# Performance work log

Hardware: AMD Instinct MI355X
Metric: run time of the kernel (lower is better)

## Reference

```python
import jax, jax.numpy as jnp
import numpy as np

SAMPLE_RATE = 48000.0
WIN_SIZE = 512   # also the FFT size (nfft = win_size in forward)
HOP_SIZE = 256   # win_size // 2, COLA with Hann
B = 128
NUM_FREQ_PTS = 96000  # 2 s RIR at 48 kHz


def _hann(n):
    # torch.hann_window default is periodic: 0.5*(1 - cos(2*pi*k/n))
    k = jnp.arange(n, dtype=jnp.float32)
    return 0.5 * (1.0 - jnp.cos(2.0 * jnp.pi * k / n))


def _stft(x, win, nfft, hop):
    # x: [B, L] real. center=False, onesided=True, not normalized.
    L = x.shape[-1]
    pad = (-L) % hop  # pad to multiple of hop, as in get_stft_torch
    if pad:
        x = jnp.pad(x, ((0, 0), (0, pad)))
    T = (x.shape[-1] - nfft) // hop + 1  # number of frames
    idx = hop * jnp.arange(T)[:, None] + jnp.arange(nfft)[None, :]  # [T, nfft]
    frames = x[:, idx] * win  # [B, T, nfft]
    return jnp.fft.rfft(frames, n=nfft, axis=-1)  # [B, T, F], F = nfft//2 + 1


def _edr_db(S):
    # S: [B, T, F] complex. EDR[m] = sum_{t>=m} |S[t]|^2  -> reverse cumsum (O(T)).
    P = jnp.abs(S) ** 2  # [B, T, F]
    edr = jnp.flip(jnp.cumsum(jnp.flip(P, axis=1), axis=1), axis=1)
    return 10.0 * jnp.log10(edr)  # db(..., is_squared=True)


def reference(target_re, target_im, ach_re, ach_im):
    n = target_re.shape[-1]
    target_rir = jnp.fft.irfft(target_re + 1j * target_im, n=n)
    ach_rir = jnp.fft.irfft(ach_re + 1j * ach_im, n=n)
    win = _hann(WIN_SIZE)
    S_t = _stft(target_rir, win, WIN_SIZE, HOP_SIZE)
    S_a = _stft(ach_rir, win, WIN_SIZE, HOP_SIZE)
    edr_t = _edr_db(S_t)
    edr_a = _edr_db(S_a)
    return jnp.sum(jnp.abs(edr_t - edr_a)) / jnp.sum(jnp.abs(edr_t))


def setup_inputs() -> dict:
    key = jax.random.key(0)
    k1, k2, k3, k4 = jax.random.split(key, 4)
    shape = (B, NUM_FREQ_PTS)
    return {
        "target_re": jax.random.normal(k1, shape, dtype=jnp.float32),
        "target_im": jax.random.normal(k2, shape, dtype=jnp.float32),
        "ach_re": jax.random.normal(k3, shape, dtype=jnp.float32),
        "ach_im": jax.random.normal(k4, shape, dtype=jnp.float32),
    }
```

## Files before the change

kernel.cpp:

```cpp
#include <hip/hip_runtime.h>
#include <math.h>

#define BATCH   128
#define NFREQ   96000
#define M_HALF  48000
#define NFRAMES 374
#define NBINS   257
#define NG      11
#define GLEN    34
#define FPW     4

#define CS1 246
#define CS2 206

#define PI_D 3.14159265358979323846

#define WAVE_SYNC() __asm__ volatile("s_waitcnt lgkmcnt(0)" ::: "memory")

__device__ __forceinline__ float2 cmulf(float2 a, float2 b) {
  return make_float2(a.x * b.x - a.y * b.y, a.x * b.y + a.y * b.x);
}

__device__ __forceinline__ void bfly4(float2 z0, float2 z1, float2 z2, float2 z3,
                                      float2& o0, float2& o1, float2& o2, float2& o3) {
  float2 e0 = make_float2(z0.x + z2.x, z0.y + z2.y);
  float2 e1 = make_float2(z0.x - z2.x, z0.y - z2.y);
  float2 e2 = make_float2(z1.x + z3.x, z1.y + z3.y);
  float2 e3 = make_float2(z1.x - z3.x, z1.y - z3.y);
  o0 = make_float2(e0.x + e2.x, e0.y + e2.y);
  o2 = make_float2(e0.x - e2.x, e0.y - e2.y);
  o1 = make_float2(e1.x + e3.y, e1.y - e3.x);
  o3 = make_float2(e1.x - e3.y, e1.y + e3.x);
}

__device__ __forceinline__ void bfly4i(float2 z0, float2 z1, float2 z2, float2 z3,
                                       float2& o0, float2& o1, float2& o2, float2& o3) {
  float2 e0 = make_float2(z0.x + z2.x, z0.y + z2.y);
  float2 e1 = make_float2(z0.x - z2.x, z0.y - z2.y);
  float2 e2 = make_float2(z1.x + z3.x, z1.y + z3.y);
  float2 e3 = make_float2(z1.x - z3.x, z1.y - z3.y);
  o0 = make_float2(e0.x + e2.x, e0.y + e2.y);
  o2 = make_float2(e0.x - e2.x, e0.y - e2.y);
  o1 = make_float2(e1.x - e3.y, e1.y + e3.x);
  o3 = make_float2(e1.x + e3.y, e1.y - e3.x);
}

#define PIDX(i) ((i) + ((i) >> 3))

__global__ void setup_kernel(float2* __restrict__ Wm, float2* __restrict__ Wpack,
                             float2* __restrict__ W512, float* __restrict__ hann,
                             float2* __restrict__ W240, float2* __restrict__ W200) {
  int i = blockIdx.x * blockDim.x + threadIdx.x;
  if (i < M_HALF) {
    double th = 2.0 * PI_D * (double)i / (double)M_HALF;
    double s, c; sincos(th, &s, &c);
    Wm[i] = make_float2((float)c, (float)s);
    double th2 = PI_D * (double)i / (double)M_HALF;
    double s2, c2; sincos(th2, &s2, &c2);
    Wpack[i] = make_float2((float)c2, (float)s2);
  }
  if (i < 512) {
    double th = -2.0 * PI_D * (double)i / 512.0;
    double s, c; sincos(th, &s, &c);
    W512[i] = make_float2((float)c, (float)s);
    hann[i] = (float)(0.5 * (1.0 - cos(2.0 * PI_D * (double)i / 512.0)));
  }
  if (i < 240) {
    double th = 2.0 * PI_D * (double)i / 240.0;
    double s, c; sincos(th, &s, &c);
    W240[i] = make_float2((float)c, (float)s);
  }
  if (i < 200) {
    double th = 2.0 * PI_D * (double)i / 200.0;
    double s, c; sincos(th, &s, &c);
    W200[i] = make_float2((float)c, (float)s);
  }
}

__global__ __launch_bounds__(256) void packT_kernel(
    const float* __restrict__ tre, const float* __restrict__ tim,
    const float* __restrict__ are, const float* __restrict__ aim,
    float2* __restrict__ Zt, const float2* __restrict__ Wpack, int b0, int c) {
  __shared__ float dRe[1600], dIm[1600], mRe[1600], mIm[1600];
  const int tid = threadIdx.x;
  const int row = blockIdx.y;
  const int base = blockIdx.x * 1600;
  const int isA = row >= c;
  const int b = b0 + (isA ? row - c : row);
  const float* rr = (isA ? are : tre) + (size_t)b * NFREQ;
  const float* ii = (isA ? aim : tim) + (size_t)b * NFREQ;
  for (int j = tid; j < 1600; j += 256) {
    dRe[j] = rr[base + j];
    dIm[j] = ii[base + j];
    int mk = M_HALF - base - j;
    mRe[j] = rr[mk];
    mIm[j] = ii[mk];
  }
  __syncthreads();
  const float sc = 1.0f / (float)M_HALF;
  float2* Zrow = Zt + (size_t)row * M_HALF;
  const int k2base = blockIdx.x * 8;
  for (int e = tid; e < 1600; e += 256) {
    int k1 = e >> 3, k2o = e & 7;
    int j = k1 + 200 * k2o;
    int k = base + j;
    float xr = dRe[j], xi = dIm[j];
    float yr = mRe[j], yi = mIm[j];
    if (k == 0) { xi = 0.f; yi = 0.f; }
    float Er = 0.5f * (xr + yr);
    float Ei = 0.5f * (xi - yi);
    float Dr = 0.5f * (xr - yr);
    float Di = 0.5f * (xi + yi);
    float2 wp = Wpack[k];
    float tr = wp.x * Dr - wp.y * Di;
    float ti = wp.x * Di + wp.y * Dr;
    Zrow[k1 * 240 + k2base + k2o] = make_float2((Er - ti) * sc, (Ei + tr) * sc);
  }
}

__global__ __launch_bounds__(256) void k1_kernel(
    const float2* __restrict__ Zt, float2* __restrict__ G,
    const float2* __restrict__ Wm, const float2* __restrict__ W240) {
  __shared__ float2 LA[8 * CS1];
  __shared__ float2 LB[8 * CS1];
  const int tid = threadIdx.x;
  const int row = blockIdx.y;
  const int K0 = blockIdx.x * 8;

  {
    const float2* Zrow = Zt + (size_t)row * M_HALF + (size_t)K0 * 240;
    for (int j = tid; j < 8 * 240; j += 256) {
      int col = j / 240, k2 = j - col * 240;
      LA[col * CS1 + k2] = Zrow[j];
    }
  }
  __syncthreads();
  for (int e = tid; e < 8 * 60; e += 256) {
    int col = e & 7, p = e >> 3;
    const float2* in = LA + col * CS1;
    float2 o0, o1, o2, o3;
    bfly4i(in[p], in[p + 60], in[p + 120], in[p + 180], o0, o1, o2, o3);
    o1 = cmulf(o1, W240[p]);
    o2 = cmulf(o2, W240[2 * p]);
    o3 = cmulf(o3, W240[3 * p]);
    float2* out = LB + col * CS1 + 4 * p;
    out[0] = o0; out[1] = o1; out[2] = o2; out[3] = o3;
  }
  __syncthreads();
  for (int e = tid; e < 8 * 60; e += 256) {
    int col = e & 7, t = e >> 3;
    int q = t & 3, p = t >> 2;
    const float2* in = LB + col * CS1;
    float2 o0, o1, o2, o3;
    bfly4i(in[q + 4 * p], in[q + 4 * (p + 15)], in[q + 4 * (p + 30)],
           in[q + 4 * (p + 45)], o0, o1, o2, o3);
    o1 = cmulf(o1, W240[4 * p]);
    o2 = cmulf(o2, W240[8 * p]);
    o3 = cmulf(o3, W240[12 * p]);
    float2* out = LA + col * CS1 + q;
    out[4 * (4 * p + 0)] = o0; out[4 * (4 * p + 1)] = o1;
    out[4 * (4 * p + 2)] = o2; out[4 * (4 * p + 3)] = o3;
  }
  __syncthreads();
  {
    float2 w15[15];
#pragma unroll
    for (int m = 0; m < 15; ++m) w15[m] = W240[16 * m];
    for (int e = tid; e < 8 * 16; e += 256) {
      int col = e & 7, q = e >> 3;
      const float2* in = LA + col * CS1 + q;
      float2 a[15];
#pragma unroll
      for (int j = 0; j < 15; ++j) a[j] = in[16 * j];
      float2* out = LB + col * CS1 + q;
#pragma unroll
      for (int u = 0; u < 15; ++u) {
        float2 acc = a[0];
#pragma unroll
        for (int j = 1; j < 15; ++j) {
          float2 w = w15[(u * j) % 15];
          acc.x += a[j].x * w.x - a[j].y * w.y;
          acc.y += a[j].x * w.y + a[j].y * w.x;
        }
        out[16 * u] = acc;
      }
    }
  }
  __syncthreads();
  {
    const int col = tid & 7;
    const int k1 = K0 + col;
    int n2 = tid >> 3;
    float2 tw = Wm[k1 * n2];
    const float2 twstep = Wm[32 * k1];
    float2* Grow = G + (size_t)row * M_HALF;
    const float2* in = LB + col * CS1;
    for (; n2 < 240; n2 += 32) {
      Grow[(size_t)n2 * 200 + k1] = cmulf(in[n2], tw);
      tw = cmulf(tw, twstep);
    }
  }
}

__global__ __launch_bounds__(256) void k2_kernel(
    const float2* __restrict__ G, float2* __restrict__ X,
    const float2* __restrict__ W200) {
  __shared__ float2 LA[8 * CS2];
  __shared__ float2 LB[8 * CS2];
  const int tid = threadIdx.x;
  const int row = blockIdx.y;
  const int N20 = blockIdx.x * 8;
  const float2* Grow = G + (size_t)row * M_HALF;

  for (int e = tid; e < 8 * 200; e += 256) {
    int n2o = e / 200;
    int k1 = e - n2o * 200;
    LA[n2o * CS2 + k1] = Grow[(size_t)(N20 + n2o) * 200 + k1];
  }
  __syncthreads();
  for (int e = tid; e < 8 * 50; e += 256) {
    int col = e & 7, p = e >> 3;
    const float2* in = LA + col * CS2;
    float2 o0, o1, o2, o3;
    bfly4i(in[p], in[p + 50], in[p + 100], in[p + 150], o0, o1, o2, o3);
    o1 = cmulf(o1, W200[p]);
    o2 = cmulf(o2, W200[2 * p]);
    o3 = cmulf(o3, W200[3 * p]);
    float2* out = LB + col * CS2 + 4 * p;
    out[0] = o0; out[1] = o1; out[2] = o2; out[3] = o3;
  }
  __syncthreads();
  {
    float2 w5[5];
#pragma unroll
    for (int m = 0; m < 5; ++m) w5[m] = W200[40 * m];
    for (int e = tid; e < 8 * 40; e += 256) {
      int col = e & 7, t = e >> 3;
      int q = t & 3, p = t >> 2;
      const float2* in = LB + col * CS2 + q;
      float2 a[5];
#pragma unroll
      for (int j = 0; j < 5; ++j) a[j] = in[4 * (p + 10 * j)];
      float2* out = LA + col * CS2 + q;
#pragma unroll
      for (int u = 0; u < 5; ++u) {
        float2 acc = a[0];
#pragma unroll
        for (int j = 1; j < 5; ++j) {
          float2 w = w5[(u * j) % 5];
          acc.x += a[j].x * w.x - a[j].y * w.y;
          acc.y += a[j].x * w.y + a[j].y * w.x;
        }
        acc = cmulf(acc, W200[4 * u * p]);
        out[4 * (5 * p + u)] = acc;
      }
    }
  }
  __syncthreads();
  {
    float2 w10[10];
#pragma unroll
    for (int m = 0; m < 10; ++m) w10[m] = W200[20 * m];
    for (int e = tid; e < 8 * 20; e += 256) {
      int col = e & 7, q = e >> 3;
      const float2* in = LA + col * CS2 + q;
      float2 a[10];
#pragma unroll
      for (int j = 0; j < 10; ++j) a[j] = in[20 * j];
      float2* out = LB + col * CS2 + q;
#pragma unroll
      for (int u = 0; u < 10; ++u) {
        float2 acc = a[0];
#pragma unroll
        for (int j = 1; j < 10; ++j) {
          float2 w = w10[(u * j) % 10];
          acc.x += a[j].x * w.x - a[j].y * w.y;
          acc.y += a[j].x * w.y + a[j].y * w.x;
        }
        out[20 * u] = acc;
      }
    }
  }
  __syncthreads();
  {
    const int n2o = tid & 7;
    float2* Xrow = X + (size_t)row * M_HALF + (N20 + n2o);
    const float2* in = LB + n2o * CS2;
    for (int n1 = tid >> 3; n1 < 200; n1 += 32)
      Xrow[240 * n1] = in[n1];
  }
}

__global__ __launch_bounds__(256) void stft256_kernel(
    const float* __restrict__ xtime, float* __restrict__ P,
    const float2* __restrict__ W512, const float* __restrict__ hann) {
  __shared__ float2 lds[4][2][288];
  const int tid = threadIdx.x;
  const int wave = tid >> 6;
  const int l = tid & 63;
  const int row = blockIdx.y;
  const int frame0 = (blockIdx.x * 4 + wave) * FPW;

  float2* Abuf = lds[wave][0];
  float2* Bbuf = lds[wave][1];

  const float2* hann2 = (const float2*)hann;
  float2 hw[4];
#pragma unroll
  for (int j = 0; j < 4; ++j) hw[j] = hann2[l + 64 * j];
  float2 t1[3], t2[3], t3[3];
  {
    int p2 = l >> 2, p3 = l >> 4;
#pragma unroll
    for (int u = 1; u <= 3; ++u) {
      t1[u - 1] = W512[2 * u * l];
      t2[u - 1] = W512[8 * u * p2];
      t3[u - 1] = W512[32 * u * p3];
    }
  }

  const float2* xrow = (const float2*)xtime + (size_t)row * 48000;

  for (int fi = 0; fi < FPW; ++fi) {
    const int fr = frame0 + fi;
    const bool active = (fr < NFRAMES);
    float2 z[4];
    if (active) {
      const float2* src = xrow + fr * 128;
#pragma unroll
      for (int j = 0; j < 4; ++j) {
        float2 v = src[l + 64 * j];
        z[j] = make_float2(v.x * hw[j].x, v.y * hw[j].y);
      }
    } else {
#pragma unroll
      for (int j = 0; j < 4; ++j) z[j] = make_float2(0.f, 0.f);
    }
    float2 o0, o1, o2, o3;
    bfly4(z[0], z[1], z[2], z[3], o0, o1, o2, o3);
    o1 = cmulf(o1, t1[0]); o2 = cmulf(o2, t1[1]); o3 = cmulf(o3, t1[2]);
    Abuf[PIDX(4 * l + 0)] = o0; Abuf[PIDX(4 * l + 1)] = o1;
    Abuf[PIDX(4 * l + 2)] = o2; Abuf[PIDX(4 * l + 3)] = o3;
    WAVE_SYNC();
    {
      int q = l & 3, p = l >> 2;
      float2 a0 = Abuf[PIDX(q + 4 * p)];
      float2 a1 = Abuf[PIDX(q + 4 * (p + 16))];
      float2 a2 = Abuf[PIDX(q + 4 * (p + 32))];
      float2 a3 = Abuf[PIDX(q + 4 * (p + 48))];
      bfly4(a0, a1, a2, a3, o0, o1, o2, o3);
      o1 = cmulf(o1, t2[0]); o2 = cmulf(o2, t2[1]); o3 = cmulf(o3, t2[2]);
      int wb = q + 16 * p;
      Bbuf[PIDX(wb)] = o0; Bbuf[PIDX(wb + 4)] = o1;
      Bbuf[PIDX(wb + 8)] = o2; Bbuf[PIDX(wb + 12)] = o3;
    }
    WAVE_SYNC();
    {
      int q = l & 15, p = l >> 4;
      float2 a0 = Bbuf[PIDX(q + 16 * p)];
      float2 a1 = Bbuf[PIDX(q + 16 * (p + 4))];
      float2 a2 = Bbuf[PIDX(q + 16 * (p + 8))];
      float2 a3 = Bbuf[PIDX(q + 16 * (p + 12))];
      bfly4(a0, a1, a2, a3, o0, o1, o2, o3);
      o1 = cmulf(o1, t3[0]); o2 = cmulf(o2, t3[1]); o3 = cmulf(o3, t3[2]);
      int wb = q + 64 * p;
      Abuf[PIDX(wb)] = o0; Abuf[PIDX(wb + 16)] = o1;
      Abuf[PIDX(wb + 32)] = o2; Abuf[PIDX(wb + 48)] = o3;
    }
    WAVE_SYNC();
    {
      float2 a0 = Abuf[PIDX(l)];
      float2 a1 = Abuf[PIDX(l + 64)];
      float2 a2 = Abuf[PIDX(l + 128)];
      float2 a3 = Abuf[PIDX(l + 192)];
      bfly4(a0, a1, a2, a3, o0, o1, o2, o3);
      Bbuf[PIDX(l)] = o0; Bbuf[PIDX(l + 64)] = o1;
      Bbuf[PIDX(l + 128)] = o2; Bbuf[PIDX(l + 192)] = o3;
    }
    WAVE_SYNC();
    if (active) {
      float* Prow = P + ((size_t)row * NFRAMES + fr) * NBINS;
      for (int k = l; k <= 256; k += 64) {
        float2 Zk = Bbuf[PIDX(k & 255)];
        float2 Zm = Bbuf[PIDX((256 - k) & 255)];
        float2 E  = make_float2(0.5f * (Zk.x + Zm.x), 0.5f * (Zk.y - Zm.y));
        float2 Op = make_float2(Zk.x - Zm.x, Zk.y + Zm.y);
        float2 Od = make_float2(0.5f * Op.y, -0.5f * Op.x);
        float2 W  = W512[k];
        float2 Xb = make_float2(E.x + W.x * Od.x - W.y * Od.y,
                                E.y + W.x * Od.y + W.y * Od.x);
        Prow[k] = Xb.x * Xb.x + Xb.y * Xb.y;
      }
    }
    WAVE_SYNC();
  }
}

__global__ __launch_bounds__(256) void edrA_kernel(const float* __restrict__ P,
                                                   float* __restrict__ part) {
  const int r = blockIdx.x;
  const int g = blockIdx.y;
  const float* Pr = P + (size_t)r * (NFRAMES * NBINS);
  for (int bin = threadIdx.x; bin < NBINS; bin += 256) {
    float s = 0.f;
    const int m0 = g * GLEN;
    for (int m = m0; m < m0 + GLEN; ++m) s += Pr[m * NBINS + bin];
    part[((size_t)r * NG + g) * NBINS + bin] = s;
  }
}

__global__ __launch_bounds__(256) void edrB_kernel(const float* __restrict__ P,
                                                   const float* __restrict__ part,
                                                   double* __restrict__ accum, int c) {
  const int b = blockIdx.x;
  const int g = blockIdx.y;
  const float* Pt = P + (size_t)b * (NFRAMES * NBINS);
  const float* Pa = P + (size_t)(b + c) * (NFRAMES * NBINS);
  const float* qt = part + (size_t)b * NG * NBINS;
  const float* qa = part + (size_t)(b + c) * NG * NBINS;
  float sn = 0.f, sd = 0.f;
  for (int bin = threadIdx.x; bin < NBINS; bin += 256) {
    float ct = 0.f, ca = 0.f;
    for (int g2 = g + 1; g2 < NG; ++g2) {
      ct += qt[g2 * NBINS + bin];
      ca += qa[g2 * NBINS + bin];
    }
    const int m0 = g * GLEN;
    for (int m = m0 + GLEN - 1; m >= m0; --m) {
      ct += Pt[m * NBINS + bin];
      ca += Pa[m * NBINS + bin];
      float lt = 10.f * log10f(ct);
      float la = 10.f * log10f(ca);
      sn += fabsf(lt - la);
      sd += fabsf(lt);
    }
  }
#pragma unroll
  for (int off = 32; off > 0; off >>= 1) {
    sn += __shfl_down(sn, off, 64);
    sd += __shfl_down(sd, off, 64);
  }
  __shared__ float wsn[4], wsd[4];
  const int wave = threadIdx.x >> 6;
  if ((threadIdx.x & 63) == 0) { wsn[wave] = sn; wsd[wave] = sd; }
  __syncthreads();
  if (threadIdx.x == 0) {
    float tn = 0.f, td = 0.f;
#pragma unroll
    for (int w = 0; w < 4; ++w) { tn += wsn[w]; td += wsd[w]; }
    int slot = (blockIdx.x * NG + blockIdx.y) & 63;
    atomicAdd(&accum[slot], (double)tn);
    atomicAdd(&accum[64 + slot], (double)td);
  }
}

__global__ void final_kernel(const double* __restrict__ accum, float* __restrict__ out) {
  double n = 0.0, d = 0.0;
  for (int i = 0; i < 64; ++i) { n += accum[i]; d += accum[64 + i]; }
  out[0] = (float)(n / d);
}

extern "C" void kernel_launch(void* const* d_in, const int* in_sizes, int n_in,
                              void* d_out, int out_size, void* d_ws, size_t ws_size,
                              hipStream_t stream) {
  const float* tre = (const float*)d_in[0];
  const float* tim = (const float*)d_in[1];
  const float* are = (const float*)d_in[2];
  const float* aim = (const float*)d_in[3];
  float* out = (float*)d_out;

  char* base = (char*)d_ws;
  size_t off = 0;
  auto take = [&](size_t bytes) -> char* {
    char* p = base + off;
    off += (bytes + 255) & ~(size_t)255;
    return p;
  };
  float2* Wm    = (float2*)take((size_t)M_HALF * sizeof(float2));
  float2* Wpack = (float2*)take((size_t)M_HALF * sizeof(float2));
  float2* W512  = (float2*)take(512 * sizeof(float2));
  float*  hann  = (float*)take(512 * sizeof(float));
  float2* W240  = (float2*)take(240 * sizeof(float2));
  float2* W200  = (float2*)take(200 * sizeof(float2));
  double* accum = (double*)take(128 * sizeof(double));
  size_t fixed = off;

  const size_t perA    = (size_t)2 * M_HALF * sizeof(float2);
  const size_t perP    = (size_t)2 * NFRAMES * NBINS * sizeof(float);
  const size_t perPart = (size_t)2 * NG * NBINS * sizeof(float);
  int c = 1;
  const int cands[8] = {128, 64, 32, 16, 8, 4, 2, 1};
  for (int ci = 0; ci < 8; ++ci) {
    size_t need = fixed + ((cands[ci] * perA + 255) & ~(size_t)255)
                        + ((cands[ci] * perP + 255) & ~(size_t)255)
                        + ((cands[ci] * perPart + 255) & ~(size_t)255);
    if (need <= ws_size) { c = cands[ci]; break; }
  }
  float2* buf1 = (float2*)take((size_t)c * perA);
  char*   BP   = take((size_t)c * perP);
  float*  part = (float*)take((size_t)c * perPart);
  float2* Zt = buf1;
  float2* X  = buf1;
  float2* G  = (float2*)BP;
  float*  P  = (float*)BP;

  setup_kernel<<<(M_HALF + 255) / 256, 256, 0, stream>>>(Wm, Wpack, W512, hann,
                                                         W240, W200);
  hipMemsetAsync(accum, 0, 128 * sizeof(double), stream);

  for (int b0 = 0; b0 < BATCH; b0 += c) {
    int rows = 2 * c;
    packT_kernel<<<dim3(30, rows), 256, 0, stream>>>(tre, tim, are, aim, Zt,
                                                     Wpack, b0, c);
    k1_kernel<<<dim3(25, rows), 256, 0, stream>>>(Zt, G, Wm, W240);
    k2_kernel<<<dim3(30, rows), 256, 0, stream>>>(G, X, W200);
    {
      dim3 grid((NFRAMES + 4 * FPW - 1) / (4 * FPW), rows);
      stft256_kernel<<<grid, 256, 0, stream>>>((const float*)X, P, W512, hann);
    }
    edrA_kernel<<<dim3(rows, NG), 256, 0, stream>>>(P, part);
    edrB_kernel<<<dim3(c, NG), 256, 0, stream>>>(P, part, accum, c);
  }
  final_kernel<<<1, 1, 0, stream>>>(accum, out);
}
```

Measured before the change: 448.0 us.

## Vectorize global memory accesses and fuse group power sums into STFT kernel

Switches packT, k1, k2 and stft loads/stores to float4 accesses. The mirrored reads in packT are also reordered into a contiguous window so they can be vectorized. The per-group partial sums are now accumulated inside the STFT kernel with atomics, which removes the edrA pass over P. The power buffer is padded to a pitch of 258 so edrB can read float2 pairs per thread. This cuts memory transactions and one kernel launch, at the cost of atomic traffic and an extra memset per batch chunk.

```diff
diff --git a/kernel.cpp b/kernel.cpp
--- a/kernel.cpp
+++ b/kernel.cpp
@@ -6,6 +6,7 @@
 #define M_HALF  48000
 #define NFRAMES 374
 #define NBINS   257
+#define PPITCH  258
 #define NG      11
 #define GLEN    34
 #define FPW     4
@@ -81,40 +82,52 @@
     const float* __restrict__ tre, const float* __restrict__ tim,
     const float* __restrict__ are, const float* __restrict__ aim,
     float2* __restrict__ Zt, const float2* __restrict__ Wpack, int b0, int c) {
-  __shared__ float dRe[1600], dIm[1600], mRe[1600], mIm[1600];
+  __shared__ float4 dRe4[400], dIm4[400], mRe4[401], mIm4[401];
+  float* dRe = (float*)dRe4;
+  float* dIm = (float*)dIm4;
+  float* mRe = (float*)mRe4;
+  float* mIm = (float*)mIm4;
   const int tid = threadIdx.x;
   const int row = blockIdx.y;
   const int base = blockIdx.x * 1600;
+  const int moff = M_HALF - base - 1600;
   const int isA = row >= c;
   const int b = b0 + (isA ? row - c : row);
   const float* rr = (isA ? are : tre) + (size_t)b * NFREQ;
   const float* ii = (isA ? aim : tim) + (size_t)b * NFREQ;
-  for (int j = tid; j < 1600; j += 256) {
-    dRe[j] = rr[base + j];
-    dIm[j] = ii[base + j];
-    int mk = M_HALF - base - j;
-    mRe[j] = rr[mk];
-    mIm[j] = ii[mk];
+  {
+    const float4* rd = (const float4*)(rr + base);
+    const float4* id = (const float4*)(ii + base);
+    for (int v = tid; v < 400; v += 256) { dRe4[v] = rd[v]; dIm4[v] = id[v]; }
+    const float4* rm = (const float4*)(rr + moff);
+    const float4* im = (const float4*)(ii + moff);
+    for (int v = tid; v < 401; v += 256) { mRe4[v] = rm[v]; mIm4[v] = im[v]; }
   }
   __syncthreads();
   const float sc = 1.0f / (float)M_HALF;
   float2* Zrow = Zt + (size_t)row * M_HALF;
   const int k2base = blockIdx.x * 8;
-  for (int e = tid; e < 1600; e += 256) {
-    int k1 = e >> 3, k2o = e & 7;
-    int j = k1 + 200 * k2o;
-    int k = base + j;
-    float xr = dRe[j], xi = dIm[j];
-    float yr = mRe[j], yi = mIm[j];
-    if (k == 0) { xi = 0.f; yi = 0.f; }
-    float Er = 0.5f * (xr + yr);
-    float Ei = 0.5f * (xi - yi);
-    float Dr = 0.5f * (xr - yr);
-    float Di = 0.5f * (xi + yi);
-    float2 wp = Wpack[k];
-    float tr = wp.x * Dr - wp.y * Di;
-    float ti = wp.x * Di + wp.y * Dr;
-    Zrow[k1 * 240 + k2base + k2o] = make_float2((Er - ti) * sc, (Ei + tr) * sc);
+  for (int e = tid; e < 800; e += 256) {
+    int k1 = e >> 2, k2p = e & 3;
+    float2 z[2];
+#pragma unroll
+    for (int h = 0; h < 2; ++h) {
+      int j = k1 + 200 * (2 * k2p + h);
+      int k = base + j;
+      float xr = dRe[j], xi = dIm[j];
+      float yr = mRe[1600 - j], yi = mIm[1600 - j];
+      if (k == 0) { xi = 0.f; yi = 0.f; }
+      float Er = 0.5f * (xr + yr);
+      float Ei = 0.5f * (xi - yi);
+      float Dr = 0.5f * (xr - yr);
+      float Di = 0.5f * (xi + yi);
+      float2 wp = Wpack[k];
+      float tr = wp.x * Dr - wp.y * Di;
+      float ti = wp.x * Di + wp.y * Dr;
+      z[h] = make_float2((Er - ti) * sc, (Ei + tr) * sc);
+    }
+    ((float4*)Zrow)[k1 * 120 + (k2base >> 1) + k2p] =
+        make_float4(z[0].x, z[0].y, z[1].x, z[1].y);
   }
 }
 
@@ -128,10 +141,11 @@
   const int K0 = blockIdx.x * 8;
 
   {
-    const float2* Zrow = Zt + (size_t)row * M_HALF + (size_t)K0 * 240;
-    for (int j = tid; j < 8 * 240; j += 256) {
-      int col = j / 240, k2 = j - col * 240;
-      LA[col * CS1 + k2] = Zrow[j];
+    const float4* Zrow4 = (const float4*)(Zt + (size_t)row * M_HALF + (size_t)K0 * 240);
+    for (int v = tid; v < 960; v += 256) {
+      int col = v / 120;
+      int k2 = 2 * (v - col * 120);
+      *((float4*)(LA + col * CS1 + k2)) = Zrow4[v];
     }
   }
   __syncthreads();
@@ -188,16 +202,22 @@
   }
   __syncthreads();
   {
-    const int col = tid & 7;
-    const int k1 = K0 + col;
-    int n2 = tid >> 3;
-    float2 tw = Wm[k1 * n2];
-    const float2 twstep = Wm[32 * k1];
-    float2* Grow = G + (size_t)row * M_HALF;
-    const float2* in = LB + col * CS1;
-    for (; n2 < 240; n2 += 32) {
-      Grow[(size_t)n2 * 200 + k1] = cmulf(in[n2], tw);
-      tw = cmulf(tw, twstep);
+    const int cp = tid & 3;
+    const int k1a = K0 + 2 * cp, k1b = k1a + 1;
+    const int n2_0 = tid >> 2;
+    float2 twa = Wm[k1a * n2_0];
+    float2 twb = Wm[k1b * n2_0];
+    const float2 sta = Wm[64 * k1a];
+    const float2 stb = Wm[64 * k1b];
+    float4* Grow4 = (float4*)(G + (size_t)row * M_HALF);
+    const float2* ina = LB + (2 * cp) * CS1;
+    const float2* inb = LB + (2 * cp + 1) * CS1;
+    for (int n2 = n2_0; n2 < 240; n2 += 64) {
+      float2 va = cmulf(ina[n2], twa);
+      float2 vb = cmulf(inb[n2], twb);
+      Grow4[n2 * 100 + (K0 >> 1) + cp] = make_float4(va.x, va.y, vb.x, vb.y);
+      twa = cmulf(twa, sta);
+      twb = cmulf(twb, stb);
     }
   }
 }
@@ -210,12 +230,14 @@
   const int tid = threadIdx.x;
   const int row = blockIdx.y;
   const int N20 = blockIdx.x * 8;
-  const float2* Grow = G + (size_t)row * M_HALF;
-
-  for (int e = tid; e < 8 * 200; e += 256) {
-    int n2o = e / 200;
-    int k1 = e - n2o * 200;
-    LA[n2o * CS2 + k1] = Grow[(size_t)(N20 + n2o) * 200 + k1];
+
+  {
+    const float4* Grow4 = (const float4*)(G + (size_t)row * M_HALF + (size_t)N20 * 200);
+    for (int v = tid; v < 800; v += 256) {
+      int n2o = v / 100;
+      int k1 = 2 * (v - n2o * 100);
+      *((float4*)(LA + n2o * CS2 + k1)) = Grow4[v];
+    }
   }
   __syncthreads();
   for (int e = tid; e < 8 * 50; e += 256) {
@@ -283,16 +305,21 @@
   }
   __syncthreads();
   {
-    const int n2o = tid & 7;
-    float2* Xrow = X + (size_t)row * M_HALF + (N20 + n2o);
-    const float2* in = LB + n2o * CS2;
-    for (int n1 = tid >> 3; n1 < 200; n1 += 32)
-      Xrow[240 * n1] = in[n1];
+    const int np = tid & 3;
+    const int n1_0 = tid >> 2;
+    const float2* in0 = LB + (2 * np) * CS2;
+    const float2* in1 = LB + (2 * np + 1) * CS2;
+    float4* Xrow4 = (float4*)(X + (size_t)row * M_HALF);
+    for (int n1 = n1_0; n1 < 200; n1 += 64) {
+      float2 v0 = in0[n1], v1 = in1[n1];
+      Xrow4[(N20 >> 1) + np + 120 * n1] = make_float4(v0.x, v0.y, v1.x, v1.y);
+    }
   }
 }
 
 __global__ __launch_bounds__(256) void stft256_kernel(
     const float* __restrict__ xtime, float* __restrict__ P,
+    float* __restrict__ part,
     const float2* __restrict__ W512, const float* __restrict__ hann) {
   __shared__ float2 lds[4][2][288];
   const int tid = threadIdx.x;
@@ -304,10 +331,8 @@
   float2* Abuf = lds[wave][0];
   float2* Bbuf = lds[wave][1];
 
-  const float2* hann2 = (const float2*)hann;
-  float2 hw[4];
-#pragma unroll
-  for (int j = 0; j < 4; ++j) hw[j] = hann2[l + 64 * j];
+  const float4 hh0 = ((const float4*)hann)[l];
+  const float4 hh1 = ((const float4*)hann)[l + 64];
   float2 t1[3], t2[3], t3[3];
   {
     int p2 = l >> 2, p3 = l >> 4;
@@ -320,27 +345,29 @@
   }
 
   const float2* xrow = (const float2*)xtime + (size_t)row * 48000;
+  float acc[5] = {0.f, 0.f, 0.f, 0.f, 0.f};
 
   for (int fi = 0; fi < FPW; ++fi) {
     const int fr = frame0 + fi;
-    const bool active = (fr < NFRAMES);
-    float2 z[4];
-    if (active) {
-      const float2* src = xrow + fr * 128;
-#pragma unroll
-      for (int j = 0; j < 4; ++j) {
-        float2 v = src[l + 64 * j];
-        z[j] = make_float2(v.x * hw[j].x, v.y * hw[j].y);
-      }
-    } else {
-#pragma unroll
-      for (int j = 0; j < 4; ++j) z[j] = make_float2(0.f, 0.f);
-    }
+    if (fr >= NFRAMES) break;
+    {
+      const float4* src4 = (const float4*)(xrow + fr * 128);
+      float4 v0 = src4[l];
+      float4 v1 = src4[l + 64];
+      v0.x *= hh0.x; v0.y *= hh0.y; v0.z *= hh0.z; v0.w *= hh0.w;
+      v1.x *= hh1.x; v1.y *= hh1.y; v1.z *= hh1.z; v1.w *= hh1.w;
+      ((float4*)Bbuf)[l] = v0;
+      ((float4*)Bbuf)[l + 64] = v1;
+    }
+    WAVE_SYNC();
     float2 o0, o1, o2, o3;
-    bfly4(z[0], z[1], z[2], z[3], o0, o1, o2, o3);
-    o1 = cmulf(o1, t1[0]); o2 = cmulf(o2, t1[1]); o3 = cmulf(o3, t1[2]);
-    Abuf[PIDX(4 * l + 0)] = o0; Abuf[PIDX(4 * l + 1)] = o1;
-    Abuf[PIDX(4 * l + 2)] = o2; Abuf[PIDX(4 * l + 3)] = o3;
+    {
+      float2 z0 = Bbuf[l], z1 = Bbuf[l + 64], z2 = Bbuf[l + 128], z3 = Bbuf[l + 192];
+      bfly4(z0, z1, z2, z3, o0, o1, o2, o3);
+      o1 = cmulf(o1, t1[0]); o2 = cmulf(o2, t1[1]); o3 = cmulf(o3, t1[2]);
+      Abuf[PIDX(4 * l + 0)] = o0; Abuf[PIDX(4 * l + 1)] = o1;
+      Abuf[PIDX(4 * l + 2)] = o2; Abuf[PIDX(4 * l + 3)] = o3;
+    }
     WAVE_SYNC();
     {
       int q = l & 3, p = l >> 2;
@@ -378,9 +405,10 @@
       Bbuf[PIDX(l + 128)] = o2; Bbuf[PIDX(l + 192)] = o3;
     }
     WAVE_SYNC();
-    if (active) {
-      float* Prow = P + ((size_t)row * NFRAMES + fr) * NBINS;
-      for (int k = l; k <= 256; k += 64) {
+    {
+      float* Prow = P + ((size_t)row * NFRAMES + fr) * PPITCH;
+      int j = 0;
+      for (int k = l; k <= 256; k += 64, ++j) {
         float2 Zk = Bbuf[PIDX(k & 255)];
         float2 Zm = Bbuf[PIDX((256 - k) & 255)];
         float2 E  = make_float2(0.5f * (Zk.x + Zm.x), 0.5f * (Zk.y - Zm.y));
@@ -389,48 +417,66 @@
         float2 W  = W512[k];
         float2 Xb = make_float2(E.x + W.x * Od.x - W.y * Od.y,
                                 E.y + W.x * Od.y + W.y * Od.x);
-        Prow[k] = Xb.x * Xb.x + Xb.y * Xb.y;
+        float pwr = Xb.x * Xb.x + Xb.y * Xb.y;
+        Prow[k] = pwr;
+        acc[j] += pwr;
       }
+      bool flush = (((fr + 1) % GLEN) == 0) || (fi == FPW - 1) || (fr == NFRAMES - 1);
+      if (flush) {
+        int g = fr / GLEN;
+        float* prow = part + ((size_t)row * NG + g) * PPITCH;
+        int j2 = 0;
+        for (int k = l; k <= 256; k += 64, ++j2) {
+          atomicAdd(&prow[k], acc[j2]);
+          acc[j2] = 0.f;
+        }
+      }
     }
     WAVE_SYNC();
   }
 }
 
-__global__ __launch_bounds__(256) void edrA_kernel(const float* __restrict__ P,
-                                                   float* __restrict__ part) {
-  const int r = blockIdx.x;
-  const int g = blockIdx.y;
-  const float* Pr = P + (size_t)r * (NFRAMES * NBINS);
-  for (int bin = threadIdx.x; bin < NBINS; bin += 256) {
-    float s = 0.f;
-    const int m0 = g * GLEN;
-    for (int m = m0; m < m0 + GLEN; ++m) s += Pr[m * NBINS + bin];
-    part[((size_t)r * NG + g) * NBINS + bin] = s;
-  }
-}
-
-__global__ __launch_bounds__(256) void edrB_kernel(const float* __restrict__ P,
+__global__ __launch_bounds__(192) void edrB_kernel(const float* __restrict__ P,
                                                    const float* __restrict__ part,
                                                    double* __restrict__ accum, int c) {
   const int b = blockIdx.x;
   const int g = blockIdx.y;
-  const float* Pt = P + (size_t)b * (NFRAMES * NBINS);
-  const float* Pa = P + (size_t)(b + c) * (NFRAMES * NBINS);
-  const float* qt = part + (size_t)b * NG * NBINS;
-  const float* qa = part + (size_t)(b + c) * NG * NBINS;
+  const int tid = threadIdx.x;
+  const float* Pt = P + (size_t)b * (NFRAMES * PPITCH);
+  const float* Pa = P + (size_t)(b + c) * (NFRAMES * PPITCH);
+  const float* qt = part + (size_t)b * NG * PPITCH;
+  const float* qa = part + (size_t)(b + c) * NG * PPITCH;
   float sn = 0.f, sd = 0.f;
-  for (int bin = threadIdx.x; bin < NBINS; bin += 256) {
+  if (tid < 128) {
+    const int bin = 2 * tid;
+    float2 ct = make_float2(0.f, 0.f), ca = make_float2(0.f, 0.f);
+    for (int g2 = g + 1; g2 < NG; ++g2) {
+      float2 vt = *(const float2*)(qt + g2 * PPITCH + bin);
+      float2 va = *(const float2*)(qa + g2 * PPITCH + bin);
+      ct.x += vt.x; ct.y += vt.y; ca.x += va.x; ca.y += va.y;
+    }
+    const int m0 = g * GLEN;
+    for (int m = m0 + GLEN - 1; m >= m0; --m) {
+      float2 vt = *(const float2*)(Pt + m * PPITCH + bin);
+      float2 va = *(const float2*)(Pa + m * PPITCH + bin);
+      ct.x += vt.x; ct.y += vt.y; ca.x += va.x; ca.y += va.y;
+      float lt0 = 10.f * log10f(ct.x), la0 = 10.f * log10f(ca.x);
+      float lt1 = 10.f * log10f(ct.y), la1 = 10.f * log10f(ca.y);
+      sn += fabsf(lt0 - la0) + fabsf(lt1 - la1);
+      sd += fabsf(lt0) + fabsf(lt1);
+    }
+  } else if (tid == 128) {
+    const int bin = 256;
     float ct = 0.f, ca = 0.f;
     for (int g2 = g + 1; g2 < NG; ++g2) {
-      ct += qt[g2 * NBINS + bin];
-      ca += qa[g2 * NBINS + bin];
+      ct += qt[g2 * PPITCH + bin];
+      ca += qa[g2 * PPITCH + bin];
     }
     const int m0 = g * GLEN;
     for (int m = m0 + GLEN - 1; m >= m0; --m) {
-      ct += Pt[m * NBINS + bin];
-      ca += Pa[m * NBINS + bin];
-      float lt = 10.f * log10f(ct);
-      float la = 10.f * log10f(ca);
+      ct += Pt[m * PPITCH + bin];
+      ca += Pa[m * PPITCH + bin];
+      float lt = 10.f * log10f(ct), la = 10.f * log10f(ca);
       sn += fabsf(lt - la);
       sd += fabsf(lt);
     }
@@ -440,14 +486,14 @@
     sn += __shfl_down(sn, off, 64);
     sd += __shfl_down(sd, off, 64);
   }
-  __shared__ float wsn[4], wsd[4];
-  const int wave = threadIdx.x >> 6;
-  if ((threadIdx.x & 63) == 0) { wsn[wave] = sn; wsd[wave] = sd; }
-  __syncthreads();
-  if (threadIdx.x == 0) {
+  __shared__ float wsn[3], wsd[3];
+  const int wave = tid >> 6;
+  if ((tid & 63) == 0) { wsn[wave] = sn; wsd[wave] = sd; }
+  __syncthreads();
+  if (tid == 0) {
     float tn = 0.f, td = 0.f;
 #pragma unroll
-    for (int w = 0; w < 4; ++w) { tn += wsn[w]; td += wsd[w]; }
+    for (int w = 0; w < 3; ++w) { tn += wsn[w]; td += wsd[w]; }
     int slot = (blockIdx.x * NG + blockIdx.y) & 63;
     atomicAdd(&accum[slot], (double)tn);
     atomicAdd(&accum[64 + slot], (double)td);
@@ -486,8 +532,8 @@
   size_t fixed = off;
 
   const size_t perA    = (size_t)2 * M_HALF * sizeof(float2);
-  const size_t perP    = (size_t)2 * NFRAMES * NBINS * sizeof(float);
-  const size_t perPart = (size_t)2 * NG * NBINS * sizeof(float);
+  const size_t perP    = (size_t)2 * NFRAMES * PPITCH * sizeof(float);
+  const size_t perPart = (size_t)2 * NG * PPITCH * sizeof(float);
   int c = 1;
   const int cands[8] = {128, 64, 32, 16, 8, 4, 2, 1};
   for (int ci = 0; ci < 8; ++ci) {
@@ -510,16 +556,16 @@
 
   for (int b0 = 0; b0 < BATCH; b0 += c) {
     int rows = 2 * c;
+    hipMemsetAsync(part, 0, (size_t)c * perPart, stream);
     packT_kernel<<<dim3(30, rows), 256, 0, stream>>>(tre, tim, are, aim, Zt,
                                                      Wpack, b0, c);
     k1_kernel<<<dim3(25, rows), 256, 0, stream>>>(Zt, G, Wm, W240);
     k2_kernel<<<dim3(30, rows), 256, 0, stream>>>(G, X, W200);
     {
       dim3 grid((NFRAMES + 4 * FPW - 1) / (4 * FPW), rows);
-      stft256_kernel<<<grid, 256, 0, stream>>>((const float*)X, P, W512, hann);
-    }
-    edrA_kernel<<<dim3(rows, NG), 256, 0, stream>>>(P, part);
-    edrB_kernel<<<dim3(c, NG), 256, 0, stream>>>(P, part, accum, c);
+      stft256_kernel<<<grid, 256, 0, stream>>>((const float*)X, P, part, W512, hann);
+    }
+    edrB_kernel<<<dim3(c, NG), 192, 0, stream>>>(P, part, accum, c);
   }
   final_kernel<<<1, 1, 0, stream>>>(accum, out);
 }
```

Measured after the change: 415.9 us. 7.2% less time.
